# Optimization experiments

Measured on AMD Instinct MI355X. Metric: run time of the kernel, lower is better.

Reference implementation:

```python
import jax, jax.numpy as jnp
import numpy as np

ROLLBACK = 1  # rollback_range: warp at 2**rollback finer resolution, then downsample
B, C, H, W = 2, 32, 512, 512
CIN = 3 * (C // 2) + 2  # inner module input channels


def _bilinear_warp(img, res):
    """Bilinear gather. img: [B,Cc,Hh,Ww]; res: [B,Hh,Ww,2] pixel offsets (x,y).
    Samples img at (x+res_x, y+res_y) with zero padding outside."""
    Bb, Cc, Hh, Ww = img.shape
    gy, gx = jnp.meshgrid(jnp.arange(Hh, dtype=img.dtype),
                          jnp.arange(Ww, dtype=img.dtype), indexing='ij')
    sx = gx[None] + res[..., 0]  # [B,Hh,Ww]
    sy = gy[None] + res[..., 1]
    x0 = jnp.floor(sx); y0 = jnp.floor(sy)
    wx = sx - x0; wy = sy - y0

    def gather(yi, xi):
        inb = ((yi >= 0) & (yi < Hh) & (xi >= 0) & (xi < Ww)).astype(img.dtype)
        yc = jnp.clip(yi, 0, Hh - 1).astype(jnp.int32)
        xc = jnp.clip(xi, 0, Ww - 1).astype(jnp.int32)
        v = jax.vmap(lambda im, y, x: im[:, y, x])(img, yc, xc)  # [B,Cc,Hh,Ww]
        return v * inb[:, None]

    v00 = gather(y0, x0);     v01 = gather(y0, x0 + 1)
    v10 = gather(y0 + 1, x0); v11 = gather(y0 + 1, x0 + 1)
    wx = wx[:, None]; wy = wy[:, None]  # broadcast over channels
    return (v00 * (1 - wy) * (1 - wx) + v01 * (1 - wy) * wx
            + v10 * wy * (1 - wx) + v11 * wy * wx)


def _resize_img(img, f):  # [B,Cc,Hh,Ww] bilinear spatial resize
    Bb, Cc, Hh, Ww = img.shape
    return jax.image.resize(img, (Bb, Cc, int(Hh * f), int(Ww * f)), 'bilinear')


def _resize_res(res, f):  # [B,Hh,Ww,2]; pixel-unit values scale with resolution
    Bb, Hh, Ww, _ = res.shape
    return jax.image.resize(res, (Bb, int(Hh * f), int(Ww * f), 2), 'bilinear') * f


def res_warp_img(img, res, rollback):
    if rollback > 0:
        f = 2 ** rollback
        out = _bilinear_warp(_resize_img(img, f), _resize_res(res, f))
        return _resize_img(out, 1.0 / f)
    return _bilinear_warp(img, res)


def res_warp_res(res_a, res_b, rollback):
    # warp residual field a (treated as a 2-channel image, values in pixel units) by b
    if rollback > 0:
        f = 2 ** rollback
        a = _resize_res(res_a, f); b = _resize_res(res_b, f)
        out = jnp.transpose(_bilinear_warp(jnp.transpose(a, (0, 3, 1, 2)), b), (0, 2, 3, 1))
        return _resize_res(out, 1.0 / f)
    out = _bilinear_warp(jnp.transpose(res_a, (0, 3, 1, 2)), res_b)
    return jnp.transpose(out, (0, 2, 3, 1))


def combine_residuals(res_a, res_b, rollback):
    # flow composition: apply a then b
    return res_b + res_warp_res(res_a, res_b, rollback)


def _conv3x3(x, w, b):
    y = jax.lax.conv_general_dilated(x, w, (1, 1), 'SAME',
                                     dimension_numbers=('NCHW', 'OIHW', 'NCHW'))
    return y + b[None, :, None, None]


def setup_inputs() -> dict:
    key = jax.random.key(0)
    k1, k2, k3 = jax.random.split(key, 3)
    x = jax.random.normal(k1, (B, C, H, W), dtype=jnp.float32)
    res = jax.random.normal(k2, (B, 2, H, W), dtype=jnp.float32)  # ~1px flow
    W_inner = jax.random.normal(k3, (2, CIN, 3, 3), dtype=jnp.float32) * 0.02
    b_inner = jnp.zeros((2,), dtype=jnp.float32)
    return {"x": x, "res": res, "W_inner": W_inner, "b_inner": b_inner, "level": 0}


def reference(x, res, W_inner, b_inner, level):
    res_hw = jnp.transpose(res, (0, 2, 3, 1))  # [B,H,W,2]
    nf = x.shape[1]
    src, tgt = x[:, :nf // 2], x[:, nf // 2:]
    warped_tgt = res_warp_img(tgt, res_hw, ROLLBACK)
    bundle = jnp.concatenate([src, tgt, warped_tgt, res], axis=1)  # [B,3C/2+2,H,W]
    adj = _conv3x3(bundle, W_inner, b_inner)  # hindsight_adjustment [B,2,H,W]
    # mode == 'combine_res': state['down'][level]['input'] = combined residual
    new_res = combine_residuals(res_hw, jnp.transpose(adj, (0, 2, 3, 1)), ROLLBACK)
    hindsight_warped_tgt = res_warp_img(tgt, new_res, ROLLBACK)
    return jnp.concatenate([src, hindsight_warped_tgt], axis=1)  # [B,C,H,W]
```

## Files before the change

kernel.cpp:

```cpp
#include <hip/hip_runtime.h>
#include <hip/hip_bf16.h>
#include <cstdint>
#include <cstddef>

#define HW   512
#define HW2  1024
#define SZ   (512 * 512)
#define NPT  (34 * 34)
#define K_PTS 5

struct UpTap { int i0, i1; float w0, w1; };

__device__ __forceinline__ UpTap up_tap(int i) {
  UpTap t;
  int k = i >> 1;
  if ((i & 1) == 0) {
    t.i0 = k - 1; t.i1 = k; t.w0 = 0.25f; t.w1 = 0.75f;
    if (k == 0) { t.i0 = 0; t.w0 = 0.0f; t.w1 = 1.0f; }
  } else {
    t.i0 = k; t.i1 = k + 1; t.w0 = 0.75f; t.w1 = 0.25f;
    if (k == HW - 1) { t.i1 = HW - 1; t.w0 = 1.0f; t.w1 = 0.0f; }
  }
  return t;
}

__device__ __forceinline__ float up_at(const float* __restrict__ plane, int yi, int xi) {
  UpTap ty = up_tap(yi), tx = up_tap(xi);
  const float* r0 = plane + (size_t)ty.i0 * HW;
  const float* r1 = plane + (size_t)ty.i1 * HW;
  float v00 = r0[tx.i0], v01 = r0[tx.i1];
  float v10 = r1[tx.i0], v11 = r1[tx.i1];
  return ty.w0 * (tx.w0 * v00 + tx.w1 * v01) + ty.w1 * (tx.w0 * v10 + tx.w1 * v11);
}

__device__ __forceinline__ void axis_taps(float s, int& base, float& w0, float& w1, float& w2) {
  float f0 = floorf(s);
  int i0 = (int)f0;
  float fr = s - f0;
  int b = (i0 & 1) ? (i0 >> 1) : (i0 >> 1) - 1;
  b = b < 0 ? 0 : (b > (HW - 3) ? (HW - 3) : b);
  float w[3] = {0.0f, 0.0f, 0.0f};
  if ((unsigned)i0 < (unsigned)HW2) {
    UpTap t = up_tap(i0);
    w[t.i0 - b] += (1.0f - fr) * t.w0;
    w[t.i1 - b] += (1.0f - fr) * t.w1;
  }
  if ((unsigned)(i0 + 1) < (unsigned)HW2) {
    UpTap t = up_tap(i0 + 1);
    w[t.i0 - b] += fr * t.w0;
    w[t.i1 - b] += fr * t.w1;
  }
  base = b; w0 = w[0]; w1 = w[1]; w2 = w[2];
}

__global__ void copy_src_kernel(const float* __restrict__ x, float* __restrict__ out) {
  const size_t half = (size_t)16 * SZ;
  const size_t nvec = half / 4;
  size_t i = (size_t)blockIdx.x * blockDim.x + threadIdx.x;
  if (i < 2 * nvec) {
    size_t b = i / nvec, j = i % nvec;
    const float4* s = (const float4*)(x + b * 2 * half);
    float4* d = (float4*)(out + b * 2 * half);
    d[j] = s[j];
  }
}

struct PtTaps {
  int   off;
  float wy0, wy1, wy2, wx0, wx1, wx2;
};

__device__ __forceinline__ void compute_taps(const float* __restrict__ fx,
                                             const float* __restrict__ fy,
                                             int gx0, int gy0, int tid,
                                             PtTaps (&pt)[K_PTS]) {
  #pragma unroll
  for (int i = 0; i < K_PTS; ++i) {
    int p = tid + i * 256;
    pt[i].off = 0;
    pt[i].wy0 = pt[i].wy1 = pt[i].wy2 = 0.0f;
    pt[i].wx0 = pt[i].wx1 = pt[i].wx2 = 0.0f;
    if (p < NPT) {
      int ry = p / 34, rx = p % 34;
      int yy = gy0 + ry, xx = gx0 + rx;
      if ((unsigned)yy < (unsigned)HW2 && (unsigned)xx < (unsigned)HW2) {
        float sx = (float)xx + 2.0f * up_at(fx, yy, xx);
        float sy = (float)yy + 2.0f * up_at(fy, yy, xx);
        int bx, by;
        axis_taps(sx, bx, pt[i].wx0, pt[i].wx1, pt[i].wx2);
        axis_taps(sy, by, pt[i].wy0, pt[i].wy1, pt[i].wy2);
        pt[i].off = by * HW + bx;
      }
    }
  }
}

__device__ __forceinline__ float eval_taps(const float* __restrict__ plane, const PtTaps& t) {
  const float* p0 = plane + t.off;
  float r0 = t.wx0 * p0[0]        + t.wx1 * p0[1]          + t.wx2 * p0[2];
  float r1 = t.wx0 * p0[HW]       + t.wx1 * p0[HW + 1]     + t.wx2 * p0[HW + 2];
  float r2 = t.wx0 * p0[2 * HW]   + t.wx1 * p0[2 * HW + 1] + t.wx2 * p0[2 * HW + 2];
  return t.wy0 * r0 + t.wy1 * r1 + t.wy2 * r2;
}

__global__ void warp_img_kernel(const float* __restrict__ x,
                                const float* __restrict__ res,
                                float* __restrict__ out)
{
  __shared__ float s_tile0[NPT];
  __shared__ float s_tile1[NPT];

  const int b = blockIdx.z;
  const int tx0 = blockIdx.x * 16, ty0 = blockIdx.y * 16;
  const int gx0 = tx0 * 2 - 1, gy0 = ty0 * 2 - 1;
  const int tid = threadIdx.x;

  const float* resx = res + (size_t)b * 2 * SZ;
  const float* resy = resx + SZ;

  PtTaps pt[K_PTS];
  compute_taps(resx, resy, gx0, gy0, tid, pt);

  const int ly = tid >> 4, lx = tid & 15;
  const int oy = ty0 + ly, ox = tx0 + lx;
  const float RW[4] = {0.25f, 0.75f, 0.75f, 0.25f};
  float wy[4], wx[4];
  float sumy = 0.f, sumx = 0.f;
  #pragma unroll
  for (int d = 0; d < 4; ++d) {
    int g = 2 * oy - 1 + d;
    wy[d] = ((unsigned)g < (unsigned)HW2) ? RW[d] : 0.0f; sumy += wy[d];
    g = 2 * ox - 1 + d;
    wx[d] = ((unsigned)g < (unsigned)HW2) ? RW[d] : 0.0f; sumx += wx[d];
  }
  const float inv = 1.0f / (sumy * sumx);

  for (int c = 0; c < 16; c += 2) {
    const float* plane0 = x + ((size_t)b * 32 + 16 + c) * SZ;
    const float* plane1 = plane0 + SZ;
    #pragma unroll
    for (int i = 0; i < K_PTS; ++i) {
      int p = tid + i * 256;
      if (p < NPT) {
        s_tile0[p] = eval_taps(plane0, pt[i]);
        s_tile1[p] = eval_taps(plane1, pt[i]);
      }
    }
    __syncthreads();
    float acc0 = 0.0f, acc1 = 0.0f;
    #pragma unroll
    for (int dy = 0; dy < 4; ++dy) {
      float r0 = 0.0f, r1 = 0.0f;
      const int base = (2 * ly + dy) * 34 + 2 * lx;
      #pragma unroll
      for (int dx = 0; dx < 4; ++dx) {
        r0 += wx[dx] * s_tile0[base + dx];
        r1 += wx[dx] * s_tile1[base + dx];
      }
      acc0 += wy[dy] * r0;
      acc1 += wy[dy] * r1;
    }
    size_t o = (((size_t)b * 32 + 16 + c) * HW + oy) * HW + ox;
    out[o] = acc0 * inv;
    out[o + SZ] = acc1 * inv;
    __syncthreads();
  }
}

__global__ void conv_kernel(const float* __restrict__ x,
                            const float* __restrict__ warped,
                            const float* __restrict__ res,
                            const float* __restrict__ Wc,
                            const float* __restrict__ bc,
                            float* __restrict__ adj)
{
  __shared__ float sw[900];
  const int tid = threadIdx.y * 16 + threadIdx.x;
  for (int i = tid; i < 900; i += 256) sw[i] = Wc[i];
  __syncthreads();

  const int b = blockIdx.z;
  const int oy = blockIdx.y * 16 + threadIdx.y;
  const int ox = blockIdx.x * 16 + threadIdx.x;

  float acc0 = bc[0];
  float acc1 = bc[1];

  for (int ic = 0; ic < 50; ++ic) {
    const float* w0 = &sw[ic * 9];
    const float* w1 = &sw[450 + ic * 9];
    const float* plane;
    if (ic < 32)      plane = x      + ((size_t)b * 32 + ic) * SZ;
    else if (ic < 48) plane = warped + ((size_t)b * 32 + 16 + (ic - 32)) * SZ;
    else              plane = res    + ((size_t)b * 2 + (ic - 48)) * SZ;
    #pragma unroll
    for (int ky = 0; ky < 3; ++ky) {
      int yy = oy + ky - 1;
      bool yok = (unsigned)yy < (unsigned)HW;
      #pragma unroll
      for (int kx = 0; kx < 3; ++kx) {
        int xx = ox + kx - 1;
        float v = 0.0f;
        if (yok && (unsigned)xx < (unsigned)HW)
          v = plane[(size_t)yy * HW + xx];
        acc0 += v * w0[ky * 3 + kx];
        acc1 += v * w1[ky * 3 + kx];
      }
    }
  }
  adj[((size_t)b * 2 + 0) * SZ + (size_t)oy * HW + ox] = acc0;
  adj[((size_t)b * 2 + 1) * SZ + (size_t)oy * HW + ox] = acc1;
}

__global__ void new_res_kernel(const float* __restrict__ res,
                               const float* __restrict__ adj,
                               float* __restrict__ nres)
{
  __shared__ float s_tile0[NPT];
  __shared__ float s_tile1[NPT];

  const int b = blockIdx.z;
  const int tx0 = blockIdx.x * 16, ty0 = blockIdx.y * 16;
  const int gx0 = tx0 * 2 - 1, gy0 = ty0 * 2 - 1;
  const int tid = threadIdx.x;

  const float* adjx = adj + (size_t)b * 2 * SZ;
  const float* adjy = adjx + SZ;

  PtTaps pt[K_PTS];
  compute_taps(adjx, adjy, gx0, gy0, tid, pt);

  const int ly = tid >> 4, lx = tid & 15;
  const int oy = ty0 + ly, ox = tx0 + lx;
  const float RW[4] = {0.25f, 0.75f, 0.75f, 0.25f};
  float wy[4], wx[4];
  float sumy = 0.f, sumx = 0.f;
  #pragma unroll
  for (int d = 0; d < 4; ++d) {
    int g = 2 * oy - 1 + d;
    wy[d] = ((unsigned)g < (unsigned)HW2) ? RW[d] : 0.0f; sumy += wy[d];
    g = 2 * ox - 1 + d;
    wx[d] = ((unsigned)g < (unsigned)HW2) ? RW[d] : 0.0f; sumx += wx[d];
  }
  const float inv = 1.0f / (sumy * sumx);

  const float* plane0 = res + (size_t)b * 2 * SZ;
  const float* plane1 = plane0 + SZ;
  #pragma unroll
  for (int i = 0; i < K_PTS; ++i) {
    int p = tid + i * 256;
    if (p < NPT) {
      s_tile0[p] = eval_taps(plane0, pt[i]);
      s_tile1[p] = eval_taps(plane1, pt[i]);
    }
  }
  __syncthreads();
  float acc0 = 0.0f, acc1 = 0.0f;
  #pragma unroll
  for (int dy = 0; dy < 4; ++dy) {
    float r0 = 0.0f, r1 = 0.0f;
    const int base = (2 * ly + dy) * 34 + 2 * lx;
    #pragma unroll
    for (int dx = 0; dx < 4; ++dx) {
      r0 += wx[dx] * s_tile0[base + dx];
      r1 += wx[dx] * s_tile1[base + dx];
    }
    acc0 += wy[dy] * r0;
    acc1 += wy[dy] * r1;
  }
  size_t o = ((size_t)b * 2) * SZ + (size_t)oy * HW + ox;
  nres[o]      = acc0 * inv + adjx[(size_t)oy * HW + ox];
  nres[o + SZ] = acc1 * inv + adjy[(size_t)oy * HW + ox];
}

extern "C" void kernel_launch(void* const* d_in, const int* in_sizes, int n_in,
                              void* d_out, int out_size, void* d_ws, size_t ws_size,
                              hipStream_t stream) {
  const float* x   = (const float*)d_in[0];
  const float* res = (const float*)d_in[1];
  const float* Wc  = (const float*)d_in[2];
  const float* bc  = (const float*)d_in[3];
  float* out = (float*)d_out;

  float* adj  = (float*)d_ws;
  float* nres = adj + (size_t)2 * 2 * SZ;

  {
    const size_t nvec = 2 * ((size_t)16 * SZ / 4);
    copy_src_kernel<<<dim3((unsigned)((nvec + 255) / 256)), dim3(256), 0, stream>>>(x, out);
  }

  dim3 tile_grid(32, 32, 2);

  warp_img_kernel<<<tile_grid, dim3(256), 0, stream>>>(x, res, out);

  conv_kernel<<<tile_grid, dim3(16, 16), 0, stream>>>(x, out, res, Wc, bc, adj);

  new_res_kernel<<<tile_grid, dim3(256), 0, stream>>>(res, adj, nres);

  warp_img_kernel<<<tile_grid, dim3(256), 0, stream>>>(x, nres, out);
}
```

Measured before the change: 418.2 us.

## Stage source tiles in shared memory for the warp gather

The warp and new-residual kernels now stage a 36x36 source window, with a margin of 9, of two channel planes into shared memory as interleaved float2. Tap points whose 3x3 footprint falls inside that window are evaluated from LDS, and any outliers fall back to global reads. In the warp kernel the next channel pair is staged right after the tile sync, so staging overlaps the downsample stage. This targets the repeated uncoalesced global gathers (18 per point per channel pair), at the cost of extra LDS, extra staging loads and a divergent fallback path for large flows.

After: 411.7 us. About the same (-1.6%).

```diff
diff --git a/kernel.cpp b/kernel.cpp
--- a/kernel.cpp
+++ b/kernel.cpp
@@ -8,6 +8,9 @@
 #define SZ   (512 * 512)
 #define NPT  (34 * 34)
 #define K_PTS 5
+#define SRCW 36
+#define NSRC (SRCW * SRCW)
+#define MARG 9
 
 struct UpTap { int i0, i1; float w0, w1; };
 
@@ -66,18 +69,18 @@
 }
 
 struct PtTaps {
-  int   off;
+  int   locoff;
   float wy0, wy1, wy2, wx0, wx1, wx2;
 };
 
 __device__ __forceinline__ void compute_taps(const float* __restrict__ fx,
                                              const float* __restrict__ fy,
-                                             int gx0, int gy0, int tid,
+                                             int gx0, int gy0, int xo, int yo, int tid,
                                              PtTaps (&pt)[K_PTS]) {
   #pragma unroll
   for (int i = 0; i < K_PTS; ++i) {
     int p = tid + i * 256;
-    pt[i].off = 0;
+    pt[i].locoff = 0;
     pt[i].wy0 = pt[i].wy1 = pt[i].wy2 = 0.0f;
     pt[i].wx0 = pt[i].wx1 = pt[i].wx2 = 0.0f;
     if (p < NPT) {
@@ -89,37 +92,96 @@
         int bx, by;
         axis_taps(sx, bx, pt[i].wx0, pt[i].wx1, pt[i].wx2);
         axis_taps(sy, by, pt[i].wy0, pt[i].wy1, pt[i].wy2);
-        pt[i].off = by * HW + bx;
+        int rx_ = bx - xo, ry_ = by - yo;
+        if ((unsigned)rx_ <= (unsigned)(SRCW - 3) && (unsigned)ry_ <= (unsigned)(SRCW - 3))
+          pt[i].locoff = ry_ * SRCW + rx_;
+        else
+          pt[i].locoff = ~(by * HW + bx);
       }
     }
   }
 }
 
-__device__ __forceinline__ float eval_taps(const float* __restrict__ plane, const PtTaps& t) {
-  const float* p0 = plane + t.off;
+__device__ __forceinline__ void stage_pair(const float* __restrict__ p0,
+                                           const float* __restrict__ p1,
+                                           float2* __restrict__ s_src,
+                                           int xo, int yo, int tid) {
+  #pragma unroll
+  for (int i = 0; i < 6; ++i) {
+    int p = tid + i * 256;
+    if (p < NSRC) {
+      int r = p / SRCW, c = p % SRCW;
+      int gy = yo + r; gy = gy < 0 ? 0 : (gy > HW - 1 ? HW - 1 : gy);
+      int gx = xo + c; gx = gx < 0 ? 0 : (gx > HW - 1 ? HW - 1 : gx);
+      size_t o = (size_t)gy * HW + gx;
+      s_src[p] = make_float2(p0[o], p1[o]);
+    }
+  }
+}
+
+__device__ __forceinline__ float eval3_global(const float* __restrict__ pl, int off, const PtTaps& t) {
+  const float* p0 = pl + off;
   float r0 = t.wx0 * p0[0]        + t.wx1 * p0[1]          + t.wx2 * p0[2];
   float r1 = t.wx0 * p0[HW]       + t.wx1 * p0[HW + 1]     + t.wx2 * p0[HW + 2];
   float r2 = t.wx0 * p0[2 * HW]   + t.wx1 * p0[2 * HW + 1] + t.wx2 * p0[2 * HW + 2];
   return t.wy0 * r0 + t.wy1 * r1 + t.wy2 * r2;
 }
 
+__device__ __forceinline__ void eval_round(const float2* __restrict__ s_src,
+                                           float2* __restrict__ s_tile,
+                                           const float* __restrict__ plane0,
+                                           const float* __restrict__ plane1,
+                                           const PtTaps (&pt)[K_PTS], int tid) {
+  #pragma unroll
+  for (int i = 0; i < K_PTS; ++i) {
+    int p = tid + i * 256;
+    if (p < NPT) {
+      const PtTaps t = pt[i];
+      float a0, a1;
+      if (t.locoff >= 0) {
+        const float2* s = s_src + t.locoff;
+        float2 v00 = s[0],        v01 = s[1],            v02 = s[2];
+        float2 v10 = s[SRCW],     v11 = s[SRCW + 1],     v12 = s[SRCW + 2];
+        float2 v20 = s[2 * SRCW], v21 = s[2 * SRCW + 1], v22 = s[2 * SRCW + 2];
+        float r00 = t.wx0 * v00.x + t.wx1 * v01.x + t.wx2 * v02.x;
+        float r10 = t.wx0 * v10.x + t.wx1 * v11.x + t.wx2 * v12.x;
+        float r20 = t.wx0 * v20.x + t.wx1 * v21.x + t.wx2 * v22.x;
+        float r01 = t.wx0 * v00.y + t.wx1 * v01.y + t.wx2 * v02.y;
+        float r11 = t.wx0 * v10.y + t.wx1 * v11.y + t.wx2 * v12.y;
+        float r21 = t.wx0 * v20.y + t.wx1 * v21.y + t.wx2 * v22.y;
+        a0 = t.wy0 * r00 + t.wy1 * r10 + t.wy2 * r20;
+        a1 = t.wy0 * r01 + t.wy1 * r11 + t.wy2 * r21;
+      } else {
+        int off = ~t.locoff;
+        a0 = eval3_global(plane0, off, t);
+        a1 = eval3_global(plane1, off, t);
+      }
+      s_tile[p] = make_float2(a0, a1);
+    }
+  }
+}
+
 __global__ void warp_img_kernel(const float* __restrict__ x,
                                 const float* __restrict__ res,
                                 float* __restrict__ out)
 {
-  __shared__ float s_tile0[NPT];
-  __shared__ float s_tile1[NPT];
+  __shared__ float2 s_src[NSRC];
+  __shared__ float2 s_tile[NPT];
 
   const int b = blockIdx.z;
   const int tx0 = blockIdx.x * 16, ty0 = blockIdx.y * 16;
   const int gx0 = tx0 * 2 - 1, gy0 = ty0 * 2 - 1;
+  const int xo = tx0 - MARG, yo = ty0 - MARG;
   const int tid = threadIdx.x;
 
   const float* resx = res + (size_t)b * 2 * SZ;
   const float* resy = resx + SZ;
+  const float* tgt  = x + ((size_t)b * 32 + 16) * SZ;
+
+  stage_pair(tgt, tgt + SZ, s_src, xo, yo, tid);
 
   PtTaps pt[K_PTS];
-  compute_taps(resx, resy, gx0, gy0, tid, pt);
+  compute_taps(resx, resy, gx0, gy0, xo, yo, tid, pt);
 
   const int ly = tid >> 4, lx = tid & 15;
   const int oy = ty0 + ly, ox = tx0 + lx;
@@ -135,18 +197,16 @@
   }
   const float inv = 1.0f / (sumy * sumx);
 
+  __syncthreads();
+
   for (int c = 0; c < 16; c += 2) {
-    const float* plane0 = x + ((size_t)b * 32 + 16 + c) * SZ;
-    const float* plane1 = plane0 + SZ;
-    #pragma unroll
-    for (int i = 0; i < K_PTS; ++i) {
-      int p = tid + i * 256;
-      if (p < NPT) {
-        s_tile0[p] = eval_taps(plane0, pt[i]);
-        s_tile1[p] = eval_taps(plane1, pt[i]);
-      }
-    }
+    const float* plane0 = tgt + (size_t)c * SZ;
+    eval_round(s_src, s_tile, plane0, plane0 + SZ, pt, tid);
     __syncthreads();
+
+    if (c < 14)
+      stage_pair(plane0 + 2 * SZ, plane0 + 3 * SZ, s_src, xo, yo, tid);
+
     float acc0 = 0.0f, acc1 = 0.0f;
     #pragma unroll
     for (int dy = 0; dy < 4; ++dy) {
@@ -154,8 +214,9 @@
       const int base = (2 * ly + dy) * 34 + 2 * lx;
       #pragma unroll
       for (int dx = 0; dx < 4; ++dx) {
-        r0 += wx[dx] * s_tile0[base + dx];
-        r1 += wx[dx] * s_tile1[base + dx];
+        float2 v = s_tile[base + dx];
+        r0 += wx[dx] * v.x;
+        r1 += wx[dx] * v.y;
       }
       acc0 += wy[dy] * r0;
       acc1 += wy[dy] * r1;
@@ -216,19 +277,24 @@
                                const float* __restrict__ adj,
                                float* __restrict__ nres)
 {
-  __shared__ float s_tile0[NPT];
-  __shared__ float s_tile1[NPT];
+  __shared__ float2 s_src[NSRC];
+  __shared__ float2 s_tile[NPT];
 
   const int b = blockIdx.z;
   const int tx0 = blockIdx.x * 16, ty0 = blockIdx.y * 16;
   const int gx0 = tx0 * 2 - 1, gy0 = ty0 * 2 - 1;
+  const int xo = tx0 - MARG, yo = ty0 - MARG;
   const int tid = threadIdx.x;
 
   const float* adjx = adj + (size_t)b * 2 * SZ;
   const float* adjy = adjx + SZ;
+  const float* res0 = res + (size_t)b * 2 * SZ;
+  const float* res1 = res0 + SZ;
+
+  stage_pair(res0, res1, s_src, xo, yo, tid);
 
   PtTaps pt[K_PTS];
-  compute_taps(adjx, adjy, gx0, gy0, tid, pt);
+  compute_taps(adjx, adjy, gx0, gy0, xo, yo, tid, pt);
 
   const int ly = tid >> 4, lx = tid & 15;
   const int oy = ty0 + ly, ox = tx0 + lx;
@@ -244,17 +310,10 @@
   }
   const float inv = 1.0f / (sumy * sumx);
 
-  const float* plane0 = res + (size_t)b * 2 * SZ;
-  const float* plane1 = plane0 + SZ;
-  #pragma unroll
-  for (int i = 0; i < K_PTS; ++i) {
-    int p = tid + i * 256;
-    if (p < NPT) {
-      s_tile0[p] = eval_taps(plane0, pt[i]);
-      s_tile1[p] = eval_taps(plane1, pt[i]);
-    }
-  }
   __syncthreads();
+  eval_round(s_src, s_tile, res0, res1, pt, tid);
+  __syncthreads();
+
   float acc0 = 0.0f, acc1 = 0.0f;
   #pragma unroll
   for (int dy = 0; dy < 4; ++dy) {
@@ -262,8 +321,9 @@
     const int base = (2 * ly + dy) * 34 + 2 * lx;
     #pragma unroll
     for (int dx = 0; dx < 4; ++dx) {
-      r0 += wx[dx] * s_tile0[base + dx];
-      r1 += wx[dx] * s_tile1[base + dx];
+      float2 v = s_tile[base + dx];
+      r0 += wx[dx] * v.x;
+      r1 += wx[dx] * v.y;
     }
     acc0 += wy[dy] * r0;
     acc1 += wy[dy] * r1;
```
